# Kernel tuning notes

Hardware: AMD Instinct MI355X
Metric: run time of the kernel (lower is better)

The kernel has to match this reference:

```python
import jax, jax.numpy as jnp
import numpy as np

TWO_PI = 2.0 * np.pi
SIGMA = 25.0  # marginal_prob_std sigma


def marginal_prob_std(t):
    # std(t) = sqrt((sigma^{2t} - 1) / (2 ln sigma)) for VE-SDE
    return jnp.sqrt((SIGMA ** (2.0 * t) - 1.0) / (2.0 * np.log(SIGMA)))


def edge_conv(x, src, dst, W1, b1, W2, b2, num_nodes):
    # PyG EdgeConv: msg = mlp(cat([x_i, x_j - x_i])), x_i = x[dst], x_j = x[src];
    # scatter-max over dst. First linear split so concat is never materialized:
    # cat([x_i, x_j - x_i]) @ W1 = x_i @ (Wa - Wb) + x_j @ Wb
    d = x.shape[-1]
    Wa, Wb = W1[:d], W1[d:]
    h_center = x @ (Wa - Wb)        # [N, H]
    h_nbr = x @ Wb                  # [N, H]
    e = jax.nn.relu(h_center[dst] + h_nbr[src] + b1)  # [E, H]
    e = e @ W2 + b2                 # [E, out]
    return jax.ops.segment_max(e, dst, num_segments=num_nodes)


def setup_inputs() -> dict:
    N, E, B, H, EM = 50000, 500000, 1024, 128, 64
    CLS, SD, GD, WD = 10, 4, 2, 2
    key = jax.random.key(0)
    ks = jax.random.split(key, 32)

    def lin(k, fi, fo):
        return jax.random.normal(k, (fi, fo), jnp.float32) / np.sqrt(fi)

    inp = {
        "t": jax.random.uniform(ks[0], (N, 1), jnp.float32, 1e-3, 1.0),
        "obj_x": jax.random.normal(ks[1], (N, SD), jnp.float32),
        "obj_geo": jax.random.normal(ks[2], (N, GD), jnp.float32),
        "wall": jax.random.normal(ks[3], (B, WD), jnp.float32),
        "category": jax.random.randint(ks[4], (N,), 0, CLS),
        "batch_idx": jnp.sort(jax.random.randint(ks[5], (N,), 0, B)),
        "src": jax.random.randint(ks[6], (E,), 0, N),
        "dst": jnp.tile(jnp.arange(N), E // N),  # every node receives edges
        "embed_W": jax.random.normal(ks[7], (CLS, EM), jnp.float32),
        "gfp_W": jax.random.normal(ks[8], (EM // 2,), jnp.float32) * 30.0,
        "sW": lin(ks[9], EM, EM), "sb": jnp.zeros((EM,), jnp.float32),
        "w1": lin(ks[10], WD, EM), "wb1": jnp.zeros((EM,), jnp.float32),
        "w2": lin(ks[11], EM, EM), "wb2": jnp.zeros((EM,), jnp.float32),
        "i1": lin(ks[12], SD + GD, H), "ib1": jnp.zeros((H,), jnp.float32),
        "i2": lin(ks[13], H, H), "ib2": jnp.zeros((H,), jnp.float32),
        "m1W1": lin(ks[14], 2 * (H + 3 * EM), H), "m1b1": jnp.zeros((H,), jnp.float32),
        "m1W2": lin(ks[15], H, H), "m1b2": jnp.zeros((H,), jnp.float32),
        "m2W1": lin(ks[16], 2 * (H + 3 * EM), H), "m2b1": jnp.zeros((H,), jnp.float32),
        "m2W2": lin(ks[17], H, SD), "m2b2": jnp.zeros((SD,), jnp.float32),
    }
    return inp


def reference(t, obj_x, obj_geo, wall, category, batch_idx, src, dst,
              embed_W, gfp_W, sW, sb, w1, wb1, w2, wb2,
              i1, ib1, i2, ib2, m1W1, m1b1, m1W2, m1b2,
              m2W1, m2b1, m2W2, m2b2):
    N = obj_x.shape[0]
    # conditioning features
    class_feat = jax.nn.relu(embed_W[category])                       # [N, EM]
    tv = t[:, 0]                                                      # [N]
    x_proj = tv[:, None] * gfp_W[None, :] * TWO_PI                    # [N, EM/2]
    gfp = jnp.concatenate([jnp.sin(x_proj), jnp.cos(x_proj)], axis=-1)
    sigma_feat = jax.nn.relu(gfp @ sW + sb)                           # [N, EM]
    wall_h = jax.nn.relu(jax.nn.relu(wall @ w1 + wb1) @ w2 + wb2)     # [B, EM]
    wall_feat = wall_h[batch_idx]                                     # [N, EM]
    cond = jnp.concatenate([class_feat, sigma_feat, wall_feat], axis=-1)

    # init encoder
    xin = jnp.concatenate([obj_x, obj_geo], axis=-1)                  # [N, 6]
    init = jax.nn.relu(jax.nn.relu(xin @ i1 + ib1) @ i2 + ib2)        # [N, H]

    # main backbone: two EdgeConvs with conditioning concat
    x = jnp.concatenate([init, cond], axis=-1)                        # [N, H+3EM]
    x = jax.nn.relu(edge_conv(x, src, dst, m1W1, m1b1, m1W2, m1b2, N))
    x = jnp.concatenate([x, cond], axis=-1)                           # [N, H+3EM]
    x = edge_conv(x, src, dst, m2W1, m2b1, m2W2, m2b2, N)             # [N, 4]

    return x / (marginal_prob_std(t) + 1e-7)
```

## Files before the change

### kernel.cpp

```cpp
#include <hip/hip_runtime.h>
#include <hip/hip_bf16.h>
#include <math.h>

#define NTHREADS 256
#define TWO_PI_F 6.28318530717958647692f
#define LOG_SIGMA 3.2188758248682006f

typedef unsigned short u16;
typedef unsigned int u32;
typedef short bf16x8 __attribute__((ext_vector_type(8)));
typedef float f32x4 __attribute__((ext_vector_type(4)));

#define MFMA(a, b, c) __builtin_amdgcn_mfma_f32_16x16x32_bf16((a), (b), (c), 0, 0, 0)

__device__ __forceinline__ u16 f2b(float f) {
  __hip_bfloat16 h = __float2bfloat16(f);
  return __builtin_bit_cast(u16, h);
}
__device__ __forceinline__ u32 pk2(float lo, float hi) {
  return (u32)f2b(lo) | ((u32)f2b(hi) << 16);
}
__device__ __forceinline__ float blo(u32 u) { return __uint_as_float(u << 16); }
__device__ __forceinline__ float bhi(u32 u) { return __uint_as_float(u & 0xffff0000u); }

__global__ __launch_bounds__(256) void prep_kernel(
    const float* __restrict__ m1W2, const float* __restrict__ m1W1,
    const float* __restrict__ m2W1, const float* __restrict__ sW,
    const float* __restrict__ i1, const float* __restrict__ i2,
    u16* __restrict__ m1W2t, u16* __restrict__ Wc1t, u16* __restrict__ Wc2t,
    u16* __restrict__ sWt, u16* __restrict__ i1t, u16* __restrict__ i2t) {
  int idx = blockIdx.x * 256 + threadIdx.x;
  if (idx < 16384) {
    int n = idx >> 7, k = idx & 127;
    m1W2t[idx] = f2b(m1W2[k * 128 + n]);
  } else if (idx < 98304) {
    int j = idx - 16384;
    int n = j / 320, k = j - n * 320;
    float v = (n < 128) ? (m1W1[k * 128 + n] - m1W1[(320 + k) * 128 + n])
                        : m1W1[(320 + k) * 128 + (n - 128)];
    Wc1t[j] = f2b(v);
  } else if (idx < 180224) {
    int j = idx - 98304;
    int n = j / 320, k = j - n * 320;
    float v = (n < 128) ? (m2W1[k * 128 + n] - m2W1[(320 + k) * 128 + n])
                        : m2W1[(320 + k) * 128 + (n - 128)];
    Wc2t[j] = f2b(v);
  } else if (idx < 184320) {
    int j = idx - 180224;
    int n = j >> 6, k = j & 63;
    sWt[j] = f2b(sW[k * 64 + n]);
  } else if (idx < 188416) {
    int j = idx - 184320;
    int n = j >> 5, k = j & 31;
    i1t[j] = (k < 6) ? f2b(i1[k * 128 + n]) : (u16)0;
  } else if (idx < 204800) {
    int j = idx - 188416;
    int n = j >> 7, k = j & 127;
    i2t[j] = f2b(i2[k * 128 + n]);
  }
}

__global__ void wall_kernel(const float* __restrict__ wall,
                            const float* __restrict__ w1, const float* __restrict__ wb1,
                            const float* __restrict__ w2, const float* __restrict__ wb2,
                            float* __restrict__ wall_h) {
  __shared__ float h1[64];
  int b = blockIdx.x;
  int f = threadIdx.x;
  float v = wall[b * 2 + 0] * w1[f] + wall[b * 2 + 1] * w1[64 + f] + wb1[f];
  h1[f] = fmaxf(v, 0.f);
  __syncthreads();
  float acc = wb2[f];
  for (int k = 0; k < 64; ++k) acc = fmaf(h1[k], w2[k * 64 + f], acc);
  wall_h[b * 64 + f] = fmaxf(acc, 0.f);
}

__global__ __launch_bounds__(256) void node_kernel(
    const float* __restrict__ t, const float* __restrict__ obj_x,
    const float* __restrict__ obj_geo,
    const int* __restrict__ category, const int* __restrict__ batch_idx,
    const float* __restrict__ embed_W, const float* __restrict__ gfp_W,
    const u16* __restrict__ sWt, const float* __restrict__ sb,
    const u16* __restrict__ i1t, const float* __restrict__ ib1,
    const u16* __restrict__ i2t, const float* __restrict__ ib2,
    const u16* __restrict__ Wc1t, const float* __restrict__ m1b1,
    const float* __restrict__ wall_h,
    float* __restrict__ hc1, u16* __restrict__ hn1,
    u16* __restrict__ cond_bf, int N) {
  __shared__ u16 xb[64 * 328];
  __shared__ u16 ab[64 * 136];
  __shared__ float t_s[64];
  __shared__ int cat_s[64];
  __shared__ int bid_s[64];

  const int tid = threadIdx.x;
  const int base = blockIdx.x * 64;
  const int wave = tid >> 6, lane = tid & 63;
  const int ln16 = lane & 15, q8 = lane >> 4;

  bf16x8 bs0 = *(const bf16x8*)(sWt + (size_t)((wave * 16 + ln16) * 64) + q8 * 8);
  bf16x8 bs1 = *(const bf16x8*)(sWt + (size_t)((wave * 16 + ln16) * 64) + 32 + q8 * 8);
  bf16x8 bh[2];
#pragma unroll
  for (int nt = 0; nt < 2; ++nt)
    bh[nt] = *(const bf16x8*)(i1t + (size_t)((wave * 32 + nt * 16 + ln16) * 32) + q8 * 8);

  if (tid < 64) {
    int node = min(base + tid, N - 1);
    t_s[tid] = t[node];
    cat_s[tid] = category[node];
    bid_s[tid] = batch_idx[node];
  }
  __syncthreads();

  for (int idx = tid; idx < 64 * 32; idx += NTHREADS) {
    int row = idx >> 5, k = idx & 31;
    float xp = t_s[row] * gfp_W[k] * TWO_PI_F;
    float s, c;
    sincosf(xp, &s, &c);
    ab[row * 136 + k] = f2b(s);
    ab[row * 136 + 32 + k] = f2b(c);
  }
  for (int idx = tid; idx < 64 * 64; idx += NTHREADS) {
    int row = idx >> 6, f = idx & 63;
    xb[row * 328 + 128 + f] = f2b(fmaxf(embed_W[cat_s[row] * 64 + f], 0.f));
    xb[row * 328 + 256 + f] = f2b(wall_h[bid_s[row] * 64 + f]);
  }
  __syncthreads();

  f32x4 cs[4];
#pragma unroll
  for (int mt = 0; mt < 4; ++mt) cs[mt] = (f32x4)0.f;
#pragma unroll
  for (int mt = 0; mt < 4; ++mt) {
    bf16x8 a0 = *(const bf16x8*)&ab[(mt * 16 + ln16) * 136 + q8 * 8];
    cs[mt] = MFMA(a0, bs0, cs[mt]);
  }
#pragma unroll
  for (int mt = 0; mt < 4; ++mt) {
    bf16x8 a1 = *(const bf16x8*)&ab[(mt * 16 + ln16) * 136 + 32 + q8 * 8];
    cs[mt] = MFMA(a1, bs1, cs[mt]);
  }
  __syncthreads();

  {
    int col = wave * 16 + ln16;
    float bias = sb[col];
#pragma unroll
    for (int mt = 0; mt < 4; ++mt)
#pragma unroll
      for (int r = 0; r < 4; ++r)
        xb[(mt * 16 + q8 * 4 + r) * 328 + 192 + col] = f2b(fmaxf(cs[mt][r] + bias, 0.f));
  }
  for (int idx = tid; idx < 64 * 32; idx += NTHREADS) {
    int row = idx >> 5, k = idx & 31;
    int node = min(base + row, N - 1);
    float v = (k < 4) ? obj_x[node * 4 + k] : ((k < 6) ? obj_geo[node * 2 + (k - 4)] : 0.f);
    ab[row * 136 + k] = f2b(v);
  }
  __syncthreads();

  for (int idx = tid; idx < 64 * 24; idx += NTHREADS) {
    int row = idx / 24, q = idx - row * 24;
    int node = base + row;
    if (node < N)
      *(uint4*)&cond_bf[(size_t)node * 192 + q * 8] = *(uint4*)&xb[row * 328 + 128 + q * 8];
  }

  f32x4 ch[2][4];
#pragma unroll
  for (int nt = 0; nt < 2; ++nt)
#pragma unroll
    for (int mt = 0; mt < 4; ++mt) ch[nt][mt] = (f32x4)0.f;
#pragma unroll
  for (int mt = 0; mt < 4; ++mt) {
    bf16x8 a = *(const bf16x8*)&ab[(mt * 16 + ln16) * 136 + q8 * 8];
#pragma unroll
    for (int nt = 0; nt < 2; ++nt) ch[nt][mt] = MFMA(a, bh[nt], ch[nt][mt]);
  }
  bf16x8 bcur2[2], bnext2[2];
#pragma unroll
  for (int nt = 0; nt < 2; ++nt)
    bcur2[nt] = *(const bf16x8*)(i2t + (size_t)((wave * 32 + nt * 16 + ln16) * 128) + q8 * 8);
  __syncthreads();
#pragma unroll
  for (int nt = 0; nt < 2; ++nt) {
    int col = wave * 32 + nt * 16 + ln16;
    float bias = ib1[col];
#pragma unroll
    for (int mt = 0; mt < 4; ++mt)
#pragma unroll
      for (int r = 0; r < 4; ++r)
        ab[(mt * 16 + q8 * 4 + r) * 136 + col] = f2b(fmaxf(ch[nt][mt][r] + bias, 0.f));
  }
  __syncthreads();

  f32x4 ci[2][4];
#pragma unroll
  for (int nt = 0; nt < 2; ++nt)
#pragma unroll
    for (int mt = 0; mt < 4; ++mt) ci[nt][mt] = (f32x4)0.f;
  for (int kt = 0; kt < 4; ++kt) {
    if (kt < 3) {
#pragma unroll
      for (int nt = 0; nt < 2; ++nt)
        bnext2[nt] = *(const bf16x8*)(i2t + (size_t)((wave * 32 + nt * 16 + ln16) * 128) +
                                      (kt + 1) * 32 + q8 * 8);
    }
#pragma unroll
    for (int mt = 0; mt < 4; ++mt) {
      bf16x8 a = *(const bf16x8*)&ab[(mt * 16 + ln16) * 136 + kt * 32 + q8 * 8];
#pragma unroll
      for (int nt = 0; nt < 2; ++nt) ci[nt][mt] = MFMA(a, bcur2[nt], ci[nt][mt]);
    }
#pragma unroll
    for (int nt = 0; nt < 2; ++nt) bcur2[nt] = bnext2[nt];
  }
#pragma unroll
  for (int nt = 0; nt < 2; ++nt) {
    int col = wave * 32 + nt * 16 + ln16;
    float bias = ib2[col];
#pragma unroll
    for (int mt = 0; mt < 4; ++mt)
#pragma unroll
      for (int r = 0; r < 4; ++r)
        xb[(mt * 16 + q8 * 4 + r) * 328 + col] = f2b(fmaxf(ci[nt][mt][r] + bias, 0.f));
  }
  __syncthreads();

  f32x4 c2[4][4];
#pragma unroll
  for (int nt = 0; nt < 4; ++nt)
#pragma unroll
    for (int mt = 0; mt < 4; ++mt) c2[nt][mt] = (f32x4)0.f;
  bf16x8 bcur[4], bnext[4];
#pragma unroll
  for (int nt = 0; nt < 4; ++nt)
    bcur[nt] = *(const bf16x8*)(Wc1t + (size_t)((wave * 64 + nt * 16 + ln16) * 320) + q8 * 8);
  for (int kt = 0; kt < 10; ++kt) {
    if (kt < 9) {
#pragma unroll
      for (int nt = 0; nt < 4; ++nt)
        bnext[nt] = *(const bf16x8*)(Wc1t + (size_t)((wave * 64 + nt * 16 + ln16) * 320) +
                                     (kt + 1) * 32 + q8 * 8);
    }
#pragma unroll
    for (int mt = 0; mt < 4; ++mt) {
      bf16x8 a = *(const bf16x8*)&xb[(mt * 16 + ln16) * 328 + kt * 32 + q8 * 8];
#pragma unroll
      for (int nt = 0; nt < 4; ++nt) c2[nt][mt] = MFMA(a, bcur[nt], c2[nt][mt]);
    }
#pragma unroll
    for (int nt = 0; nt < 4; ++nt) bcur[nt] = bnext[nt];
  }
#pragma unroll
  for (int nt = 0; nt < 4; ++nt) {
    int col = wave * 64 + nt * 16 + ln16;
#pragma unroll
    for (int mt = 0; mt < 4; ++mt)
#pragma unroll
      for (int r = 0; r < 4; ++r) {
        int node = base + mt * 16 + q8 * 4 + r;
        if (node < N) {
          if (col < 128)
            hc1[(size_t)node * 128 + col] = c2[nt][mt][r] + m1b1[col];
          else
            hn1[(size_t)node * 128 + (col - 128)] = f2b(c2[nt][mt][r]);
        }
      }
  }
}

__device__ __forceinline__ void pack_edge(u16* __restrict__ dst, const float* __restrict__ hcr,
                                          uint4 g0, uint4 g1, int ln, int kq) {
  float a[16];
  a[0] = blo(g0.x); a[1] = bhi(g0.x); a[2] = blo(g0.y); a[3] = bhi(g0.y);
  a[4] = blo(g0.z); a[5] = bhi(g0.z); a[6] = blo(g0.w); a[7] = bhi(g0.w);
  a[8] = blo(g1.x); a[9] = bhi(g1.x); a[10] = blo(g1.y); a[11] = bhi(g1.y);
  a[12] = blo(g1.z); a[13] = bhi(g1.z); a[14] = blo(g1.w); a[15] = bhi(g1.w);
#pragma unroll
  for (int i = 0; i < 16; ++i) a[i] = fmaxf(hcr[i] + a[i], 0.f);
  uint4 o0, o1;
  o0.x = pk2(a[0], a[1]); o0.y = pk2(a[2], a[3]); o0.z = pk2(a[4], a[5]); o0.w = pk2(a[6], a[7]);
  o1.x = pk2(a[8], a[9]); o1.y = pk2(a[10], a[11]); o1.z = pk2(a[12], a[13]); o1.w = pk2(a[14], a[15]);
  *(uint4*)&dst[ln * 136 + kq * 16] = o0;
  *(uint4*)&dst[ln * 136 + kq * 16 + 8] = o1;
}

__global__ __launch_bounds__(256) void edge1_kernel(
    const float* __restrict__ hc1, const u16* __restrict__ hn1,
    const u16* __restrict__ cond_bf, const int* __restrict__ src,
    const u16* __restrict__ m1W2t, const float* __restrict__ m1b2,
    const u16* __restrict__ Wc2t, const float* __restrict__ m2b1,
    float* __restrict__ hc2, u16* __restrict__ hn2, int N) {
  __shared__ u16 a_lds[2][32 * 136];
  __shared__ u16 x2_lds[32 * 328];
  __shared__ int sid[320];

  const int tid = threadIdx.x;
  const int base = blockIdx.x * 32;
  const int wave = tid >> 6, lane = tid & 63;
  const int ln16 = lane & 15, q8 = lane >> 4;

  for (int idx = tid; idx < 320; idx += NTHREADS) {
    int e = idx >> 5, n = idx & 31;
    int node = min(base + n, N - 1);
    sid[idx] = src[node + e * N];
  }
  for (int idx = tid; idx < 768; idx += NTHREADS) {
    int n = idx / 24, q = idx - n * 24;
    int node = min(base + n, N - 1);
    *(uint4*)&x2_lds[n * 328 + 128 + q * 8] = *(const uint4*)&cond_bf[(size_t)node * 192 + q * 8];
  }
  const int ln = tid >> 3, kq = tid & 7;
  const int lnode = min(base + ln, N - 1);
  float hcr[16];
#pragma unroll
  for (int q = 0; q < 4; ++q) {
    float4 v = *(const float4*)&hc1[(size_t)lnode * 128 + kq * 16 + q * 4];
    hcr[q * 4 + 0] = v.x; hcr[q * 4 + 1] = v.y; hcr[q * 4 + 2] = v.z; hcr[q * 4 + 3] = v.w;
  }
  bf16x8 bfrag[2][4];
#pragma unroll
  for (int nt = 0; nt < 2; ++nt)
#pragma unroll
    for (int kt = 0; kt < 4; ++kt)
      bfrag[nt][kt] = *(const bf16x8*)(m1W2t + (size_t)((2 * wave + nt) * 16 + ln16) * 128 +
                                       kt * 32 + q8 * 8);

  f32x4 ymax[2][2];
#pragma unroll
  for (int mt = 0; mt < 2; ++mt)
#pragma unroll
    for (int nt = 0; nt < 2; ++nt)
#pragma unroll
      for (int r = 0; r < 4; ++r) ymax[mt][nt][r] = -3.0e38f;

  __syncthreads();

  {
    int s0 = sid[ln];
    uint4 g0 = *(const uint4*)&hn1[(size_t)s0 * 128 + kq * 16];
    uint4 g1 = *(const uint4*)&hn1[(size_t)s0 * 128 + kq * 16 + 8];
    pack_edge(&a_lds[0][0], hcr, g0, g1, ln, kq);
  }
  uint4 gA0, gA1, gB0, gB1;
  {
    int s1 = sid[32 + ln];
    gA0 = *(const uint4*)&hn1[(size_t)s1 * 128 + kq * 16];
    gA1 = *(const uint4*)&hn1[(size_t)s1 * 128 + kq * 16 + 8];
    int s2 = sid[64 + ln];
    gB0 = *(const uint4*)&hn1[(size_t)s2 * 128 + kq * 16];
    gB1 = *(const uint4*)&hn1[(size_t)s2 * 128 + kq * 16 + 8];
  }
  asm volatile("s_waitcnt lgkmcnt(0)" ::: "memory");
  __builtin_amdgcn_s_barrier();

#pragma unroll 2
  for (int e = 0; e < 10; ++e) {
    const u16* abuf = &a_lds[e & 1][0];
    f32x4 c[2][2];
#pragma unroll
    for (int mt = 0; mt < 2; ++mt)
#pragma unroll
      for (int nt = 0; nt < 2; ++nt) c[mt][nt] = (f32x4)0.f;
#pragma unroll
    for (int kt = 0; kt < 4; ++kt) {
      bf16x8 a0 = *(const bf16x8*)&abuf[ln16 * 136 + kt * 32 + q8 * 8];
      bf16x8 a1 = *(const bf16x8*)&abuf[(16 + ln16) * 136 + kt * 32 + q8 * 8];
#pragma unroll
      for (int nt = 0; nt < 2; ++nt) {
        c[0][nt] = MFMA(a0, bfrag[nt][kt], c[0][nt]);
        c[1][nt] = MFMA(a1, bfrag[nt][kt], c[1][nt]);
      }
    }
#pragma unroll
    for (int mt = 0; mt < 2; ++mt)
#pragma unroll
      for (int nt = 0; nt < 2; ++nt)
#pragma unroll
        for (int r = 0; r < 4; ++r) ymax[mt][nt][r] = fmaxf(ymax[mt][nt][r], c[mt][nt][r]);

    if (e < 9) {
      if ((e & 1) == 0) {
        pack_edge(&a_lds[1][0], hcr, gA0, gA1, ln, kq);
        if (e + 3 < 10) {
          int s = sid[(e + 3) * 32 + ln];
          gA0 = *(const uint4*)&hn1[(size_t)s * 128 + kq * 16];
          gA1 = *(const uint4*)&hn1[(size_t)s * 128 + kq * 16 + 8];
        }
      } else {
        pack_edge(&a_lds[0][0], hcr, gB0, gB1, ln, kq);
        if (e + 3 < 10) {
          int s = sid[(e + 3) * 32 + ln];
          gB0 = *(const uint4*)&hn1[(size_t)s * 128 + kq * 16];
          gB1 = *(const uint4*)&hn1[(size_t)s * 128 + kq * 16 + 8];
        }
      }
      asm volatile("s_waitcnt lgkmcnt(0)" ::: "memory");
      __builtin_amdgcn_s_barrier();
    }
  }

#pragma unroll
  for (int mt = 0; mt < 2; ++mt)
#pragma unroll
    for (int nt = 0; nt < 2; ++nt) {
      int col = (2 * wave + nt) * 16 + ln16;
      float bias = m1b2[col];
#pragma unroll
      for (int r = 0; r < 4; ++r) {
        int row = mt * 16 + q8 * 4 + r;
        x2_lds[row * 328 + col] = f2b(fmaxf(ymax[mt][nt][r] + bias, 0.f));
      }
    }
  __syncthreads();

  f32x4 c2[2][4];
#pragma unroll
  for (int mt = 0; mt < 2; ++mt)
#pragma unroll
    for (int nt = 0; nt < 4; ++nt) c2[mt][nt] = (f32x4)0.f;
  bf16x8 bcur[4], bnext[4];
#pragma unroll
  for (int nt = 0; nt < 4; ++nt)
    bcur[nt] = *(const bf16x8*)(Wc2t + (size_t)((wave * 4 + nt) * 16 + ln16) * 320 + q8 * 8);
  for (int kt = 0; kt < 10; ++kt) {
    if (kt < 9) {
#pragma unroll
      for (int nt = 0; nt < 4; ++nt)
        bnext[nt] = *(const bf16x8*)(Wc2t + (size_t)((wave * 4 + nt) * 16 + ln16) * 320 +
                                     (kt + 1) * 32 + q8 * 8);
    }
    bf16x8 a0 = *(const bf16x8*)&x2_lds[ln16 * 328 + kt * 32 + q8 * 8];
    bf16x8 a1 = *(const bf16x8*)&x2_lds[(16 + ln16) * 328 + kt * 32 + q8 * 8];
#pragma unroll
    for (int nt = 0; nt < 4; ++nt) {
      c2[0][nt] = MFMA(a0, bcur[nt], c2[0][nt]);
      c2[1][nt] = MFMA(a1, bcur[nt], c2[1][nt]);
    }
#pragma unroll
    for (int nt = 0; nt < 4; ++nt) bcur[nt] = bnext[nt];
  }
#pragma unroll
  for (int mt = 0; mt < 2; ++mt)
#pragma unroll
    for (int nt = 0; nt < 4; ++nt) {
      int col = (wave * 4 + nt) * 16 + ln16;
#pragma unroll
      for (int r = 0; r < 4; ++r) {
        int row = mt * 16 + q8 * 4 + r;
        int node = base + row;
        if (node < N) {
          if (wave < 2)
            hc2[(size_t)node * 128 + col] = c2[mt][nt][r] + m2b1[col];
          else
            hn2[(size_t)node * 128 + (col - 128)] = f2b(c2[mt][nt][r]);
        }
      }
    }
}

__global__ __launch_bounds__(256) void edge2_kernel(
    const float* __restrict__ hc2, const u16* __restrict__ hn2,
    const int* __restrict__ src, const float* __restrict__ t,
    const float* __restrict__ m2W2, const float* __restrict__ m2b2,
    float* __restrict__ out, int N) {
  const int tid = threadIdx.x;
  const int base = blockIdx.x * 32;
  const int ln = tid >> 3, kq = tid & 7;
  const int node = min(base + ln, N - 1);

  float hcr[16];
#pragma unroll
  for (int q = 0; q < 4; ++q) {
    float4 v = *(const float4*)&hc2[(size_t)node * 128 + kq * 16 + q * 4];
    hcr[q * 4 + 0] = v.x; hcr[q * 4 + 1] = v.y; hcr[q * 4 + 2] = v.z; hcr[q * 4 + 3] = v.w;
  }
  float w[16][4];
#pragma unroll
  for (int i = 0; i < 16; ++i) {
    float4 v = *(const float4*)&m2W2[(kq * 16 + i) * 4];
    w[i][0] = v.x; w[i][1] = v.y; w[i][2] = v.z; w[i][3] = v.w;
  }
  float ymax[4] = {-3.0e38f, -3.0e38f, -3.0e38f, -3.0e38f};

  uint4 gA0, gA1, gB0, gB1;
  {
    int s0 = src[node];
    gA0 = *(const uint4*)&hn2[(size_t)s0 * 128 + kq * 16];
    gA1 = *(const uint4*)&hn2[(size_t)s0 * 128 + kq * 16 + 8];
    int s1 = src[node + N];
    gB0 = *(const uint4*)&hn2[(size_t)s1 * 128 + kq * 16];
    gB1 = *(const uint4*)&hn2[(size_t)s1 * 128 + kq * 16 + 8];
  }
#pragma unroll 2
  for (int e = 0; e < 10; ++e) {
    uint4 h0, h1;
    if ((e & 1) == 0) {
      h0 = gA0; h1 = gA1;
      if (e + 2 < 10) {
        int s = src[node + (e + 2) * N];
        gA0 = *(const uint4*)&hn2[(size_t)s * 128 + kq * 16];
        gA1 = *(const uint4*)&hn2[(size_t)s * 128 + kq * 16 + 8];
      }
    } else {
      h0 = gB0; h1 = gB1;
      if (e + 2 < 10) {
        int s = src[node + (e + 2) * N];
        gB0 = *(const uint4*)&hn2[(size_t)s * 128 + kq * 16];
        gB1 = *(const uint4*)&hn2[(size_t)s * 128 + kq * 16 + 8];
      }
    }
    float a[16];
    a[0] = blo(h0.x); a[1] = bhi(h0.x); a[2] = blo(h0.y); a[3] = bhi(h0.y);
    a[4] = blo(h0.z); a[5] = bhi(h0.z); a[6] = blo(h0.w); a[7] = bhi(h0.w);
    a[8] = blo(h1.x); a[9] = bhi(h1.x); a[10] = blo(h1.y); a[11] = bhi(h1.y);
    a[12] = blo(h1.z); a[13] = bhi(h1.z); a[14] = blo(h1.w); a[15] = bhi(h1.w);
    float acc[4] = {0.f, 0.f, 0.f, 0.f};
#pragma unroll
    for (int i = 0; i < 16; ++i) {
      float av = fmaxf(hcr[i] + a[i], 0.f);
#pragma unroll
      for (int j = 0; j < 4; ++j) acc[j] = fmaf(av, w[i][j], acc[j]);
    }
#pragma unroll
    for (int mask = 1; mask <= 4; mask <<= 1)
#pragma unroll
      for (int j = 0; j < 4; ++j) acc[j] += __shfl_xor(acc[j], mask);
#pragma unroll
    for (int j = 0; j < 4; ++j) ymax[j] = fmaxf(ymax[j], acc[j]);
  }
  if (kq < 4 && base + ln < N) {
    float tv = t[node];
    float mps = sqrtf((expf(2.f * tv * LOG_SIGMA) - 1.f) * (1.f / (2.f * LOG_SIGMA)));
    out[(size_t)node * 4 + kq] = (ymax[kq] + m2b2[kq]) / (mps + 1e-7f);
  }
}

extern "C" void kernel_launch(void* const* d_in, const int* in_sizes, int n_in,
                              void* d_out, int out_size, void* d_ws, size_t ws_size,
                              hipStream_t stream) {
  const float* t = (const float*)d_in[0];
  const float* obj_x = (const float*)d_in[1];
  const float* obj_geo = (const float*)d_in[2];
  const float* wall = (const float*)d_in[3];
  const int* category = (const int*)d_in[4];
  const int* batch_idx = (const int*)d_in[5];
  const int* src = (const int*)d_in[6];
  const float* embed_W = (const float*)d_in[8];
  const float* gfp_W = (const float*)d_in[9];
  const float* sW = (const float*)d_in[10];
  const float* sb = (const float*)d_in[11];
  const float* w1 = (const float*)d_in[12];
  const float* wb1 = (const float*)d_in[13];
  const float* w2 = (const float*)d_in[14];
  const float* wb2 = (const float*)d_in[15];
  const float* i1 = (const float*)d_in[16];
  const float* ib1 = (const float*)d_in[17];
  const float* i2 = (const float*)d_in[18];
  const float* ib2 = (const float*)d_in[19];
  const float* m1W1 = (const float*)d_in[20];
  const float* m1b1 = (const float*)d_in[21];
  const float* m1W2 = (const float*)d_in[22];
  const float* m1b2 = (const float*)d_in[23];
  const float* m2W1 = (const float*)d_in[24];
  const float* m2b1 = (const float*)d_in[25];
  const float* m2W2 = (const float*)d_in[26];
  const float* m2b2 = (const float*)d_in[27];
  float* out = (float*)d_out;

  const int N = in_sizes[0];
  const int B = in_sizes[3] / 2;

  char* w = (char*)d_ws;
  float* wall_h = (float*)w; w += (size_t)B * 64 * 4;
  u16* cond_bf = (u16*)w;   w += (size_t)N * 192 * 2;
  float* hc1 = (float*)w;   w += (size_t)N * 128 * 4;
  u16* hn1 = (u16*)w;       w += (size_t)N * 128 * 2;
  float* hc2 = (float*)w;   w += (size_t)N * 128 * 4;
  u16* hn2 = (u16*)w;       w += (size_t)N * 128 * 2;
  u16* m1W2t = (u16*)w;     w += (size_t)128 * 128 * 2;
  u16* Wc1t = (u16*)w;      w += (size_t)256 * 320 * 2;
  u16* Wc2t = (u16*)w;      w += (size_t)256 * 320 * 2;
  u16* sWt = (u16*)w;       w += (size_t)64 * 64 * 2;
  u16* i1t = (u16*)w;       w += (size_t)128 * 32 * 2;
  u16* i2t = (u16*)w;       w += (size_t)128 * 128 * 2;

  prep_kernel<<<dim3(800), dim3(256), 0, stream>>>(m1W2, m1W1, m2W1, sW, i1, i2,
                                                   m1W2t, Wc1t, Wc2t, sWt, i1t, i2t);
  wall_kernel<<<dim3(B), dim3(64), 0, stream>>>(wall, w1, wb1, w2, wb2, wall_h);
  node_kernel<<<dim3((N + 63) / 64), dim3(NTHREADS), 0, stream>>>(
      t, obj_x, obj_geo, category, batch_idx, embed_W, gfp_W, sWt, sb,
      i1t, ib1, i2t, ib2, Wc1t, m1b1, wall_h, hc1, hn1, cond_bf, N);
  edge1_kernel<<<dim3((N + 31) / 32), dim3(NTHREADS), 0, stream>>>(
      hc1, hn1, cond_bf, src, m1W2t, m1b2, Wc2t, m2b1, hc2, hn2, N);
  edge2_kernel<<<dim3((N + 31) / 32), dim3(NTHREADS), 0, stream>>>(
      hc2, hn2, src, t, m2W2, m2b2, out, N);
}
```

Measured before the change: 299.1 us.

## Fuse wall MLP into prep kernel and restructure edge2 gather for coalescing

The wall MLP is merged into the weight-prep kernel as extra blocks, removing one kernel launch. The edge2 kernel now loads all ten source indices up front and splits the 128-wide feature dimension into two 64-wide passes, so the eight lanes of a node read contiguous 16-byte chunks, which should coalesce better. Per-edge partial sums are kept in registers and reduced across lanes at the end, with sched_barriers to control instruction scheduling. The trade-off is higher register pressure (40 accumulators) and loading the hc2 and weight slices twice.

Result: faster. 270.0 us (median of 2 runs) (-9.7%).

```diff
diff --git a/kernel.cpp b/kernel.cpp
--- a/kernel.cpp
+++ b/kernel.cpp
@@ -23,12 +23,32 @@
 __device__ __forceinline__ float blo(u32 u) { return __uint_as_float(u << 16); }
 __device__ __forceinline__ float bhi(u32 u) { return __uint_as_float(u & 0xffff0000u); }
 
-__global__ __launch_bounds__(256) void prep_kernel(
+__global__ __launch_bounds__(256) void prep_wall_kernel(
     const float* __restrict__ m1W2, const float* __restrict__ m1W1,
     const float* __restrict__ m2W1, const float* __restrict__ sW,
     const float* __restrict__ i1, const float* __restrict__ i2,
+    const float* __restrict__ wall, const float* __restrict__ w1,
+    const float* __restrict__ wb1, const float* __restrict__ w2,
+    const float* __restrict__ wb2,
     u16* __restrict__ m1W2t, u16* __restrict__ Wc1t, u16* __restrict__ Wc2t,
-    u16* __restrict__ sWt, u16* __restrict__ i1t, u16* __restrict__ i2t) {
+    u16* __restrict__ sWt, u16* __restrict__ i1t, u16* __restrict__ i2t,
+    float* __restrict__ wall_h, int B) {
+  if (blockIdx.x >= 800) {
+    __shared__ float h1[4][64];
+    int g = threadIdx.x >> 6, f = threadIdx.x & 63;
+    int b = (blockIdx.x - 800) * 4 + g;
+    if (b < B) {
+      float v = wall[b * 2 + 0] * w1[f] + wall[b * 2 + 1] * w1[64 + f] + wb1[f];
+      h1[g][f] = fmaxf(v, 0.f);
+    }
+    __syncthreads();
+    if (b < B) {
+      float acc = wb2[f];
+      for (int k = 0; k < 64; ++k) acc = fmaf(h1[g][k], w2[k * 64 + f], acc);
+      wall_h[b * 64 + f] = fmaxf(acc, 0.f);
+    }
+    return;
+  }
   int idx = blockIdx.x * 256 + threadIdx.x;
   if (idx < 16384) {
     int n = idx >> 7, k = idx & 127;
@@ -60,21 +80,6 @@
   }
 }
 
-__global__ void wall_kernel(const float* __restrict__ wall,
-                            const float* __restrict__ w1, const float* __restrict__ wb1,
-                            const float* __restrict__ w2, const float* __restrict__ wb2,
-                            float* __restrict__ wall_h) {
-  __shared__ float h1[64];
-  int b = blockIdx.x;
-  int f = threadIdx.x;
-  float v = wall[b * 2 + 0] * w1[f] + wall[b * 2 + 1] * w1[64 + f] + wb1[f];
-  h1[f] = fmaxf(v, 0.f);
-  __syncthreads();
-  float acc = wb2[f];
-  for (int k = 0; k < 64; ++k) acc = fmaf(h1[k], w2[k * 64 + f], acc);
-  wall_h[b * 64 + f] = fmaxf(acc, 0.f);
-}
-
 __global__ __launch_bounds__(256) void node_kernel(
     const float* __restrict__ t, const float* __restrict__ obj_x,
     const float* __restrict__ obj_geo,
@@ -471,65 +476,69 @@
   const int ln = tid >> 3, kq = tid & 7;
   const int node = min(base + ln, N - 1);
 
-  float hcr[16];
-#pragma unroll
-  for (int q = 0; q < 4; ++q) {
-    float4 v = *(const float4*)&hc2[(size_t)node * 128 + kq * 16 + q * 4];
-    hcr[q * 4 + 0] = v.x; hcr[q * 4 + 1] = v.y; hcr[q * 4 + 2] = v.z; hcr[q * 4 + 3] = v.w;
-  }
-  float w[16][4];
-#pragma unroll
-  for (int i = 0; i < 16; ++i) {
-    float4 v = *(const float4*)&m2W2[(kq * 16 + i) * 4];
-    w[i][0] = v.x; w[i][1] = v.y; w[i][2] = v.z; w[i][3] = v.w;
-  }
+  int s[10];
+#pragma unroll
+  for (int e = 0; e < 10; ++e) s[e] = src[node + e * N];
+
+  float acc[10][4];
+#pragma unroll
+  for (int e = 0; e < 10; ++e)
+#pragma unroll
+    for (int j = 0; j < 4; ++j) acc[e][j] = 0.f;
+
+#pragma unroll
+  for (int p = 0; p < 2; ++p) {
+    const int d0 = p * 64 + kq * 8;
+    float hcr[8];
+    {
+      float4 v0 = *(const float4*)&hc2[(size_t)node * 128 + d0];
+      float4 v1 = *(const float4*)&hc2[(size_t)node * 128 + d0 + 4];
+      hcr[0] = v0.x; hcr[1] = v0.y; hcr[2] = v0.z; hcr[3] = v0.w;
+      hcr[4] = v1.x; hcr[5] = v1.y; hcr[6] = v1.z; hcr[7] = v1.w;
+    }
+    float w[8][4];
+#pragma unroll
+    for (int i = 0; i < 8; ++i) {
+      float4 v = *(const float4*)&m2W2[(d0 + i) * 4];
+      w[i][0] = v.x; w[i][1] = v.y; w[i][2] = v.z; w[i][3] = v.w;
+    }
+    uint4 gA = *(const uint4*)&hn2[(size_t)s[0] * 128 + d0];
+    uint4 gB = *(const uint4*)&hn2[(size_t)s[1] * 128 + d0];
+#pragma unroll
+    for (int e = 0; e < 10; ++e) {
+      uint4 h = (e & 1) ? gB : gA;
+      if (e + 2 < 10) {
+        uint4 gn = *(const uint4*)&hn2[(size_t)s[e + 2] * 128 + d0];
+        if (e & 1) gB = gn; else gA = gn;
+      }
+      float a[8];
+      a[0] = blo(h.x); a[1] = bhi(h.x); a[2] = blo(h.y); a[3] = bhi(h.y);
+      a[4] = blo(h.z); a[5] = bhi(h.z); a[6] = blo(h.w); a[7] = bhi(h.w);
+#pragma unroll
+      for (int i = 0; i < 8; ++i) {
+        float av = fmaxf(hcr[i] + a[i], 0.f);
+#pragma unroll
+        for (int j = 0; j < 4; ++j) acc[e][j] = fmaf(av, w[i][j], acc[e][j]);
+      }
+      __builtin_amdgcn_sched_barrier(0);
+    }
+  }
+
   float ymax[4] = {-3.0e38f, -3.0e38f, -3.0e38f, -3.0e38f};
-
-  uint4 gA0, gA1, gB0, gB1;
-  {
-    int s0 = src[node];
-    gA0 = *(const uint4*)&hn2[(size_t)s0 * 128 + kq * 16];
-    gA1 = *(const uint4*)&hn2[(size_t)s0 * 128 + kq * 16 + 8];
-    int s1 = src[node + N];
-    gB0 = *(const uint4*)&hn2[(size_t)s1 * 128 + kq * 16];
-    gB1 = *(const uint4*)&hn2[(size_t)s1 * 128 + kq * 16 + 8];
-  }
-#pragma unroll 2
+#pragma unroll
   for (int e = 0; e < 10; ++e) {
-    uint4 h0, h1;
-    if ((e & 1) == 0) {
-      h0 = gA0; h1 = gA1;
-      if (e + 2 < 10) {
-        int s = src[node + (e + 2) * N];
-        gA0 = *(const uint4*)&hn2[(size_t)s * 128 + kq * 16];
-        gA1 = *(const uint4*)&hn2[(size_t)s * 128 + kq * 16 + 8];
-      }
-    } else {
-      h0 = gB0; h1 = gB1;
-      if (e + 2 < 10) {
-        int s = src[node + (e + 2) * N];
-        gB0 = *(const uint4*)&hn2[(size_t)s * 128 + kq * 16];
-        gB1 = *(const uint4*)&hn2[(size_t)s * 128 + kq * 16 + 8];
-      }
-    }
-    float a[16];
-    a[0] = blo(h0.x); a[1] = bhi(h0.x); a[2] = blo(h0.y); a[3] = bhi(h0.y);
-    a[4] = blo(h0.z); a[5] = bhi(h0.z); a[6] = blo(h0.w); a[7] = bhi(h0.w);
-    a[8] = blo(h1.x); a[9] = bhi(h1.x); a[10] = blo(h1.y); a[11] = bhi(h1.y);
-    a[12] = blo(h1.z); a[13] = bhi(h1.z); a[14] = blo(h1.w); a[15] = bhi(h1.w);
-    float acc[4] = {0.f, 0.f, 0.f, 0.f};
-#pragma unroll
-    for (int i = 0; i < 16; ++i) {
-      float av = fmaxf(hcr[i] + a[i], 0.f);
-#pragma unroll
-      for (int j = 0; j < 4; ++j) acc[j] = fmaf(av, w[i][j], acc[j]);
-    }
-#pragma unroll
-    for (int mask = 1; mask <= 4; mask <<= 1)
-#pragma unroll
-      for (int j = 0; j < 4; ++j) acc[j] += __shfl_xor(acc[j], mask);
-#pragma unroll
-    for (int j = 0; j < 4; ++j) ymax[j] = fmaxf(ymax[j], acc[j]);
+    float t0 = acc[e][0], t1 = acc[e][1], t2 = acc[e][2], t3 = acc[e][3];
+#pragma unroll
+    for (int mask = 1; mask <= 4; mask <<= 1) {
+      t0 += __shfl_xor(t0, mask);
+      t1 += __shfl_xor(t1, mask);
+      t2 += __shfl_xor(t2, mask);
+      t3 += __shfl_xor(t3, mask);
+    }
+    ymax[0] = fmaxf(ymax[0], t0);
+    ymax[1] = fmaxf(ymax[1], t1);
+    ymax[2] = fmaxf(ymax[2], t2);
+    ymax[3] = fmaxf(ymax[3], t3);
   }
   if (kq < 4 && base + ln < N) {
     float tv = t[node];
@@ -587,9 +596,10 @@
   u16* i1t = (u16*)w;       w += (size_t)128 * 32 * 2;
   u16* i2t = (u16*)w;       w += (size_t)128 * 128 * 2;
 
-  prep_kernel<<<dim3(800), dim3(256), 0, stream>>>(m1W2, m1W1, m2W1, sW, i1, i2,
-                                                   m1W2t, Wc1t, Wc2t, sWt, i1t, i2t);
-  wall_kernel<<<dim3(B), dim3(64), 0, stream>>>(wall, w1, wb1, w2, wb2, wall_h);
+  int wall_blocks = (B + 3) / 4;
+  prep_wall_kernel<<<dim3(800 + wall_blocks), dim3(256), 0, stream>>>(
+      m1W2, m1W1, m2W1, sW, i1, i2, wall, w1, wb1, w2, wb2,
+      m1W2t, Wc1t, Wc2t, sWt, i1t, i2t, wall_h, B);
   node_kernel<<<dim3((N + 63) / 64), dim3(NTHREADS), 0, stream>>>(
       t, obj_x, obj_geo, category, batch_idx, embed_W, gfp_W, sWt, sb,
       i1t, ib1, i2t, ib2, Wc1t, m1b1, wall_h, hc1, hn1, cond_bf, N);
```
